# Optimization experiments

Measured on AMD Instinct MI355X. Metric: run time of the kernel, lower is better.

## Reference

```python
import jax, jax.numpy as jnp
import numpy as np

B, LC, LE, H, V = 128, 256, 257, 512, 128
PAD = 0  # padding_token_index


def lstm_cell(x, h, c, Wih, Whh, b):
    # torch LSTMCell gate order: i, f, g, o
    g = x @ Wih.T + h @ Whh.T + b
    i, f, gg, o = jnp.split(g, 4, axis=-1)
    c = jax.nn.sigmoid(f) * c + jax.nn.sigmoid(i) * jnp.tanh(gg)
    h = jax.nn.sigmoid(o) * jnp.tanh(c)
    return h, c


def setup_inputs() -> dict:
    key = jax.random.key(0)
    ks = jax.random.split(key, 32)
    p = lambda k, shape: jax.random.normal(k, shape, jnp.float32) * 0.05
    d = {
        'C_idx': jax.random.randint(ks[0], (B, LC), 0, V, dtype=jnp.int32),
        'E_idx': jax.random.randint(ks[1], (B, LE), 0, V, dtype=jnp.int32),
        'C_pad': jnp.zeros((B, LC), dtype=bool),
        'enc_Wih_f': p(ks[2], (4 * H, V)),
        'enc_Whh_f': p(ks[3], (4 * H, H)),
        'enc_b_f': p(ks[4], (4 * H,)),
        'enc_Wih_b': p(ks[5], (4 * H, V)),
        'enc_Whh_b': p(ks[6], (4 * H, H)),
        'enc_b_b': p(ks[7], (4 * H,)),
        'dec_Wih': p(ks[8], (4 * H, H + V)),
        'dec_Whh': p(ks[9], (4 * H, H)),
        'dec_b': p(ks[10], (4 * H,)),
        'Wh': p(ks[11], (H, 2 * H)),
        'Wc': p(ks[12], (H, 2 * H)),
        'Wattn': p(ks[13], (H, 2 * H)),
        'Wout': p(ks[14], (H, 3 * H)),
        'Wvocab': p(ks[15], (V, H)),
        'pg_ctx': p(ks[16], (2 * H,)),
        'pg_in': p(ks[17], (V + H,)),
        'pg_h': p(ks[18], (H,)),
        'pg_c': p(ks[19], (H,)),
        'pg_b': p(ks[20], (1,)),
    }
    return d


def _forward(C_idx, E_idx, C_pad, enc_Wih_f, enc_Whh_f, enc_b_f, enc_Wih_b, enc_Whh_b, enc_b_b,
             dec_Wih, dec_Whh, dec_b, Wh, Wc, Wattn, Wout, Wvocab,
             pg_ctx, pg_in, pg_h, pg_c, pg_b):
    C = jax.nn.one_hot(C_idx, V, dtype=jnp.float32)      # [B,LC,V]
    E_emb = jax.nn.one_hot(E_idx, V, dtype=jnp.float32)  # [B,LE,V]
    z = jnp.zeros((B, H), jnp.float32)

    xs = jnp.swapaxes(C, 0, 1)  # [LC,B,V]

    def enc_fwd(carry, x):
        h, c = lstm_cell(x, carry[0], carry[1], enc_Wih_f, enc_Whh_f, enc_b_f)
        return (h, c), h

    def enc_bwd(carry, x):
        h, c = lstm_cell(x, carry[0], carry[1], enc_Wih_b, enc_Whh_b, enc_b_b)
        return (h, c), h

    (hf, cf), Hf = jax.lax.scan(enc_fwd, (z, z), xs)
    (hb, cb), Hb = jax.lax.scan(enc_bwd, (z, z), xs[::-1])
    Hb = Hb[::-1]
    enc = jnp.swapaxes(jnp.concatenate([Hf, Hb], axis=-1), 0, 1)  # [B,LC,2H]

    # decoder init state from final encoder states (fwd;bwd concat)
    h0 = jnp.concatenate([hf, hb], axis=-1) @ Wh.T
    c0 = jnp.concatenate([cf, cb], axis=-1) @ Wc.T

    enc_proj = enc @ Wattn.T  # [B,LC,H]

    def step(carry, x_emb):
        h, c, prev_out = carry
        nin = jnp.concatenate([x_emb, prev_out], axis=1)  # [B,V+H]
        h, c = lstm_cell(nin, h, c, dec_Wih, dec_Whh, dec_b)
        scores = jnp.einsum('blh,bh->bl', enc_proj, h)
        scores = jnp.where(C_pad, -jnp.inf, scores)
        attn = jax.nn.softmax(scores, axis=1)             # [B,LC]
        ctx = jnp.einsum('bl,blh->bh', attn, enc)         # [B,2H]
        t_out = jnp.tanh(jnp.concatenate([h, ctx], axis=1) @ Wout.T)  # [B,H]
        gen = jax.nn.softmax(t_out @ Wvocab.T, axis=1)    # [B,V]
        p_gen = jax.nn.sigmoid(ctx @ pg_ctx + nin @ pg_in + h @ pg_h + c @ pg_c + pg_b[0])[:, None]
        copy_p = attn * (1.0 - p_gen)
        out = jax.vmap(lambda o, idx, a: o.at[idx].add(a))(gen * p_gen, C_idx, copy_p)
        return (h, c, t_out), out

    xs2 = jnp.swapaxes(E_emb[:, :LE - 1], 0, 1)  # teacher inputs, step 0 = start token
    _, preds = jax.lax.scan(step, (h0, c0, z), xs2)
    preds = jnp.swapaxes(preds, 0, 1)  # [B,LE-1,V]

    tgt = E_idx[:, 1:]
    nll = -jnp.take_along_axis(jnp.log(preds), tgt[..., None], axis=2)[..., 0]
    return jnp.where(tgt == PAD, 0.0, nll)  # [B,LE-1], reduction='none'


def reference(C_idx, E_idx, C_pad, enc_Wih_f, enc_Whh_f, enc_b_f, enc_Wih_b, enc_Whh_b, enc_b_b,
              dec_Wih, dec_Whh, dec_b, Wh, Wc, Wattn, Wout, Wvocab,
              pg_ctx, pg_in, pg_h, pg_c, pg_b):
    return _forward(C_idx, E_idx, C_pad, enc_Wih_f, enc_Whh_f, enc_b_f, enc_Wih_b, enc_Whh_b, enc_b_b,
                    dec_Wih, dec_Whh, dec_b, Wh, Wc, Wattn, Wout, Wvocab,
                    pg_ctx, pg_in, pg_h, pg_c, pg_b)
```

## Files before the change

### kernel.cpp

```cpp
#include <hip/hip_runtime.h>

static constexpr size_t OFF_ENC   = 0;
static constexpr size_t OFF_WGE   = 67108864;
static constexpr size_t OFF_WIHTE = 71303168;
static constexpr size_t OFF_HENC  = 72351744;
static constexpr size_t OFF_CENC  = 72876032;
static constexpr size_t OFF_WGATE = 67108864;
static constexpr size_t OFF_XDEC  = 71303168;
static constexpr size_t OFF_WATTT = 71827456;
static constexpr size_t OFF_WOUT  = 72876032;
static constexpr size_t OFF_WVOCT = 74448896;
static constexpr size_t OFF_HDEC  = 74579968;
static constexpr size_t OFF_CDEC  = 74842112;
static constexpr size_t OFF_TOUT  = 75104256;
static constexpr size_t OFF_UFB   = 75366400;
static constexpr size_t OFF_CTXF  = 75628544;
static constexpr size_t OFF_CTXP  = 75890688;
static constexpr size_t OFF_SC    = 76414976;
static constexpr size_t OFF_MSP   = 76480512;
static constexpr size_t OFF_MD    = 76482560;

__device__ __forceinline__ float sigm(float x) { return 1.f / (1.f + expf(-x)); }
__device__ __forceinline__ unsigned short f2bf(float f) {
  unsigned u = __float_as_uint(f);
  u += 0x7fffu + ((u >> 16) & 1u);
  return (unsigned short)(u >> 16);
}
__device__ __forceinline__ float bfl(unsigned w) { return __uint_as_float(w << 16); }
__device__ __forceinline__ float bfh(unsigned w) { return __uint_as_float(w & 0xffff0000u); }
__device__ __forceinline__ float bf2f(unsigned short v) { return __uint_as_float(((unsigned)v) << 16); }

#if defined(__has_builtin)
#if __has_builtin(__builtin_amdgcn_fdot2_f32_bf16)
#define HAVE_DOT2BF 1
#endif
#endif
#ifdef HAVE_DOT2BF
typedef __bf16 bf2_t __attribute__((ext_vector_type(2)));
__device__ __forceinline__ float dot2bf(unsigned w, unsigned h, float acc) {
  return __builtin_amdgcn_fdot2_f32_bf16(__builtin_bit_cast(bf2_t, w),
                                         __builtin_bit_cast(bf2_t, h), acc, false);
}
#else
__device__ __forceinline__ float dot2bf(unsigned w, unsigned h, float acc) {
  return acc + bfl(w) * bfl(h) + bfh(w) * bfh(h);
}
#endif

__global__ __launch_bounds__(256) void k_pre1(const float* __restrict__ WhhF,
                                              const float* __restrict__ WhhB,
                                              const float* __restrict__ WihF,
                                              const float* __restrict__ WihB,
                                              char* __restrict__ wsb) {
  unsigned short* WGE = (unsigned short*)(wsb + OFF_WGE);
  unsigned short* WIH = (unsigned short*)(wsb + OFF_WIHTE);
  int id = blockIdx.x * 256 + threadIdx.x, str = gridDim.x * 256;
  for (int x = id; x < 2 * 2048 * 512; x += str) {
    int dir = x >> 20, r = (x >> 9) & 2047, k = x & 511;
    const float* W = dir ? WhhB : WhhF;
    WGE[x] = f2bf(W[(size_t)r * 512 + k]);
  }
  for (int x = id; x < 2 * 128 * 2048; x += str) {
    int dir = x >> 18, v = (x >> 11) & 127, r = x & 2047;
    const float* W = dir ? WihB : WihF;
    WIH[x] = f2bf(W[(size_t)r * 128 + v]);
  }
}

__global__ __launch_bounds__(256) void k_pre2(const float* __restrict__ dWih,
                                              const float* __restrict__ dWhh,
                                              const float* __restrict__ Wattn,
                                              const float* __restrict__ Wout,
                                              const float* __restrict__ Wvoc,
                                              char* __restrict__ wsb) {
  unsigned short* WG = (unsigned short*)(wsb + OFF_WGATE);
  unsigned short* XD = (unsigned short*)(wsb + OFF_XDEC);
  unsigned short* WA = (unsigned short*)(wsb + OFF_WATTT);
  unsigned short* WO = (unsigned short*)(wsb + OFF_WOUT);
  unsigned*       WV = (unsigned*)(wsb + OFF_WVOCT);
  int id = blockIdx.x * 256 + threadIdx.x, str = gridDim.x * 256;
  for (int x = id; x < 2048 * 1024; x += str) {
    int r = x >> 10, k = x & 1023;
    float v = (k < 512) ? dWih[(size_t)r * 640 + 128 + k] : dWhh[(size_t)r * 512 + (k - 512)];
    WG[x] = f2bf(v);
  }
  for (int x = id; x < 128 * 2048; x += str) {
    int v = x >> 11, r = x & 2047;
    XD[x] = f2bf(dWih[(size_t)r * 640 + v]);
  }
  for (int x = id; x < 1024 * 512; x += str) {
    int i = x >> 9, o = x & 511;
    WA[x] = f2bf(Wattn[(size_t)o * 1024 + i]);
  }
  for (int x = id; x < 512 * 1536; x += str) WO[x] = f2bf(Wout[x]);
  for (int x = id; x < 256 * 128; x += str) {
    int kk = x >> 7, v = x & 127;
    unsigned lo = f2bf(Wvoc[(size_t)v * 512 + 2 * kk]);
    unsigned hi = f2bf(Wvoc[(size_t)v * 512 + 2 * kk + 1]);
    WV[x] = lo | (hi << 16);
  }
}

__global__ __launch_bounds__(512) void k_encs(const float* __restrict__ bF,
                                              const float* __restrict__ bB,
                                              const int* __restrict__ C_idx,
                                              char* __restrict__ wsb, int t) {
  int tau = threadIdx.x, bid = blockIdx.x;
  int b = tau & 127, slot = tau >> 7;
  int dir = bid >> 7;
  int j = __builtin_amdgcn_readfirstlane(((bid & 127) << 2) + slot);
  int dd = __builtin_amdgcn_readfirstlane(dir);
  int rp = t & 1, wp = rp ^ 1;
  const unsigned* inw = (const unsigned*)(wsb + OFF_HENC) + ((size_t)(dd * 2 + rp) * 256) * 128 + b;
  const uint4* w0 = (const uint4*)((const unsigned*)(wsb + OFF_WGE) + ((size_t)dd * 2048 + j) * 256);
  const uint4* w1 = (const uint4*)((const unsigned*)(wsb + OFF_WGE) + ((size_t)dd * 2048 + 512 + j) * 256);
  const uint4* w2 = (const uint4*)((const unsigned*)(wsb + OFF_WGE) + ((size_t)dd * 2048 + 1024 + j) * 256);
  const uint4* w3 = (const uint4*)((const unsigned*)(wsb + OFF_WGE) + ((size_t)dd * 2048 + 1536 + j) * 256);
  int l = dd ? (255 - t) : t;
  int cidx = C_idx[b * 256 + l];
  const unsigned short* xg = (const unsigned short*)(wsb + OFF_WIHTE) + ((size_t)dd * 128 + cidx) * 2048;
  const float* bias = dd ? bB : bF;
  float a0 = bias[j] + bf2f(xg[j]);
  float a1 = bias[512 + j] + bf2f(xg[512 + j]);
  float a2 = bias[1024 + j] + bf2f(xg[1024 + j]);
  float a3 = bias[1536 + j] + bf2f(xg[1536 + j]);
#pragma unroll 4
  for (int q = 0; q < 64; ++q) {
    uint4 W0 = w0[q], W1 = w1[q], W2 = w2[q], W3 = w3[q];
    unsigned i0 = inw[(q * 4 + 0) * 128], i1 = inw[(q * 4 + 1) * 128];
    unsigned i2 = inw[(q * 4 + 2) * 128], i3 = inw[(q * 4 + 3) * 128];
    a0 = dot2bf(W0.x, i0, a0); a0 = dot2bf(W0.y, i1, a0); a0 = dot2bf(W0.z, i2, a0); a0 = dot2bf(W0.w, i3, a0);
    a1 = dot2bf(W1.x, i0, a1); a1 = dot2bf(W1.y, i1, a1); a1 = dot2bf(W1.z, i2, a1); a1 = dot2bf(W1.w, i3, a1);
    a2 = dot2bf(W2.x, i0, a2); a2 = dot2bf(W2.y, i1, a2); a2 = dot2bf(W2.z, i2, a2); a2 = dot2bf(W2.w, i3, a2);
    a3 = dot2bf(W3.x, i0, a3); a3 = dot2bf(W3.y, i1, a3); a3 = dot2bf(W3.z, i2, a3); a3 = dot2bf(W3.w, i3, a3);
  }
  float ig = sigm(a0), fg = sigm(a1), gg = tanhf(a2), og = sigm(a3);
  float* cp = (float*)(wsb + OFF_CENC) + ((size_t)dir * 512 + j) * 128 + b;
  float c = fg * (*cp) + ig * gg;
  *cp = c;
  float h = og * tanhf(c);
  unsigned short hb = f2bf(h);
  ((unsigned short*)(wsb + OFF_HENC))[((((size_t)(dir * 2 + wp) * 256) + (j >> 1)) * 128 + b) * 2 + (j & 1)] = hb;
  ((unsigned short*)(wsb + OFF_ENC))[((size_t)b * 256 + l) * 1024 + dir * 512 + j] = hb;
}

__global__ __launch_bounds__(512) void k_h0(const float* __restrict__ Wh,
                                            const float* __restrict__ Wc,
                                            char* __restrict__ wsb) {
  int tau = threadIdx.x;
  int b = tau & 127, slot = tau >> 7;
  int row = __builtin_amdgcn_readfirstlane(blockIdx.x * 4 + slot);
  int sel = row >> 9, j = row & 511;
  const float* W = (sel ? Wc : Wh) + (size_t)j * 1024;
  const unsigned short* HE = (const unsigned short*)(wsb + OFF_HENC);
  const float* CE = (const float*)(wsb + OFF_CENC);
  float acc = 0.f;
  for (int k = 0; k < 1024; ++k) {
    int dir = k >> 9, k5 = k & 511;
    float in;
    if (sel == 0)
      in = bf2f(HE[((((size_t)(dir * 2 + 0) * 256) + (k5 >> 1)) * 128 + b) * 2 + (k5 & 1)]);
    else
      in = CE[((size_t)dir * 512 + k5) * 128 + b];
    acc += W[k] * in;
  }
  if (sel == 0)
    ((unsigned short*)(wsb + OFF_HDEC))[(((size_t)(j >> 1)) * 128 + b) * 2 + (j & 1)] = f2bf(acc);
  else
    ((float*)(wsb + OFF_CDEC))[(size_t)j * 128 + b] = acc;
}

__global__ __launch_bounds__(512) void k_gates(const int* __restrict__ E_idx,
                                               const float* __restrict__ db,
                                               char* __restrict__ wsb, int t) {
  __shared__ float part[2][4][128];
  int tau = threadIdx.x;
  int b = tau & 127, jslot = (tau >> 7) & 1, kh = tau >> 8;
  int j = __builtin_amdgcn_readfirstlane(blockIdx.x * 2 + jslot);
  int rp = t & 1, np = rp ^ 1;
  const unsigned* inw = (const unsigned*)(wsb + (kh ? OFF_HDEC : OFF_TOUT)) + (size_t)(kh ? np * 0 + rp : rp) * 256 * 128 + b;
  const unsigned* WG = (const unsigned*)(wsb + OFF_WGATE);
  const uint4* w0 = (const uint4*)(WG + ((size_t)(0 * 512 + j)) * 512 + kh * 256);
  const uint4* w1 = (const uint4*)(WG + ((size_t)(1 * 512 + j)) * 512 + kh * 256);
  const uint4* w2 = (const uint4*)(WG + ((size_t)(2 * 512 + j)) * 512 + kh * 256);
  const uint4* w3 = (const uint4*)(WG + ((size_t)(3 * 512 + j)) * 512 + kh * 256);
  float a0 = 0.f, a1 = 0.f, a2 = 0.f, a3 = 0.f;
#pragma unroll 4
  for (int q = 0; q < 64; ++q) {
    uint4 W0 = w0[q], W1 = w1[q], W2 = w2[q], W3 = w3[q];
    unsigned i0 = inw[(q * 4 + 0) * 128], i1 = inw[(q * 4 + 1) * 128];
    unsigned i2 = inw[(q * 4 + 2) * 128], i3 = inw[(q * 4 + 3) * 128];
    a0 = dot2bf(W0.x, i0, a0); a0 = dot2bf(W0.y, i1, a0); a0 = dot2bf(W0.z, i2, a0); a0 = dot2bf(W0.w, i3, a0);
    a1 = dot2bf(W1.x, i0, a1); a1 = dot2bf(W1.y, i1, a1); a1 = dot2bf(W1.z, i2, a1); a1 = dot2bf(W1.w, i3, a1);
    a2 = dot2bf(W2.x, i0, a2); a2 = dot2bf(W2.y, i1, a2); a2 = dot2bf(W2.z, i2, a2); a2 = dot2bf(W2.w, i3, a2);
    a3 = dot2bf(W3.x, i0, a3); a3 = dot2bf(W3.y, i1, a3); a3 = dot2bf(W3.z, i2, a3); a3 = dot2bf(W3.w, i3, a3);
  }
  if (kh == 1) { part[jslot][0][b] = a0; part[jslot][1][b] = a1; part[jslot][2][b] = a2; part[jslot][3][b] = a3; }
  __syncthreads();
  if (kh == 0) {
    int xid = E_idx[b * 257 + t];
    const unsigned short* xg = (const unsigned short*)(wsb + OFF_XDEC) + (size_t)xid * 2048;
    float g0 = a0 + part[jslot][0][b] + db[j] + bf2f(xg[j]);
    float g1 = a1 + part[jslot][1][b] + db[512 + j] + bf2f(xg[512 + j]);
    float g2 = a2 + part[jslot][2][b] + db[1024 + j] + bf2f(xg[1024 + j]);
    float g3 = a3 + part[jslot][3][b] + db[1536 + j] + bf2f(xg[1536 + j]);
    float ig = sigm(g0), fg = sigm(g1), gg = tanhf(g2), og = sigm(g3);
    float* cp = (float*)(wsb + OFF_CDEC) + (size_t)j * 128 + b;
    float c = fg * (*cp) + ig * gg;
    *cp = c;
    float h = og * tanhf(c);
    ((unsigned short*)(wsb + OFF_HDEC))[(((size_t)np * 256 + (j >> 1)) * 128 + b) * 2 + (j & 1)] = f2bf(h);
  }
}

__global__ __launch_bounds__(512) void k_u(char* __restrict__ wsb, int t) {
  int tau = threadIdx.x;
  int b = tau & 127, slot = tau >> 7;
  int i = __builtin_amdgcn_readfirstlane(blockIdx.x * 4 + slot);
  int np = (t & 1) ^ 1;
  const unsigned* inw = (const unsigned*)(wsb + OFF_HDEC) + (size_t)np * 256 * 128 + b;
  const uint4* w = (const uint4*)((const unsigned*)(wsb + OFF_WATTT) + (size_t)i * 256);
  float a = 0.f;
#pragma unroll 4
  for (int q = 0; q < 64; ++q) {
    uint4 W = w[q];
    a = dot2bf(W.x, inw[(q * 4 + 0) * 128], a);
    a = dot2bf(W.y, inw[(q * 4 + 1) * 128], a);
    a = dot2bf(W.z, inw[(q * 4 + 2) * 128], a);
    a = dot2bf(W.w, inw[(q * 4 + 3) * 128], a);
  }
  ((unsigned short*)(wsb + OFF_UFB))[(((size_t)(i >> 1)) * 128 + b) * 2 + (i & 1)] = f2bf(a);
}

__global__ __launch_bounds__(256) void k_attn(const unsigned char* __restrict__ C_pad,
                                              char* __restrict__ wsb) {
  __shared__ __align__(16) unsigned short tile[32][1024];
  __shared__ __align__(16) unsigned ulds[512];
  __shared__ float sc_l[32];
  __shared__ float p_l[32];
  __shared__ float red[4];
  int bid = blockIdx.x, tau = threadIdx.x;
  int b = bid >> 1, ch = bid & 1;
  int lane = tau & 63, wv = tau >> 6;
  const unsigned* UW = (const unsigned*)(wsb + OFF_UFB) + b;
  ulds[tau] = UW[(size_t)tau * 128];
  ulds[tau + 256] = UW[(size_t)(tau + 256) * 128];
  float mold = -3.0e38f, ssum = 0.f;
  float acc0 = 0.f, acc1 = 0.f, acc2 = 0.f, acc3 = 0.f;
  unsigned short* SCp = (unsigned short*)(wsb + OFF_SC) + (size_t)b * 256;
  int L0 = ch * 128;
  for (int sub = 0; sub < 4; ++sub) {
    const uint4* src = (const uint4*)((const unsigned short*)wsb + ((size_t)b * 256 + L0 + sub * 32) * 1024);
    __syncthreads();
#pragma unroll
    for (int it = 0; it < 16; ++it) ((uint4*)tile)[it * 256 + tau] = src[it * 256 + tau];
    __syncthreads();
    const uint4* t4 = (const uint4*)tile;
    const uint4* u4 = (const uint4*)ulds;
#pragma unroll
    for (int li = 0; li < 8; ++li) {
      int l = wv * 8 + li;
      uint4 ea = t4[l * 128 + lane * 2];
      uint4 eb = t4[l * 128 + lane * 2 + 1];
      uint4 ua = u4[lane * 2];
      uint4 ub = u4[lane * 2 + 1];
      float s = 0.f;
      s = dot2bf(ea.x, ua.x, s); s = dot2bf(ea.y, ua.y, s);
      s = dot2bf(ea.z, ua.z, s); s = dot2bf(ea.w, ua.w, s);
      s = dot2bf(eb.x, ub.x, s); s = dot2bf(eb.y, ub.y, s);
      s = dot2bf(eb.z, ub.z, s); s = dot2bf(eb.w, ub.w, s);
      for (int o = 32; o; o >>= 1) s += __shfl_xor(s, o);
      if (lane == 0) {
        int gl = L0 + sub * 32 + l;
        if (C_pad[b * 256 + gl]) s = -3.0e38f;
        sc_l[l] = s;
        SCp[gl] = f2bf(s);
      }
    }
    __syncthreads();
    if (tau < 64) {
      float v = (tau < 32) ? sc_l[tau] : -3.0e38f;
      for (int o = 32; o; o >>= 1) v = fmaxf(v, __shfl_xor(v, o));
      if (tau == 0) red[0] = v;
    }
    __syncthreads();
    float mnew = fmaxf(mold, red[0]);
    float r = expf(mold - mnew);
    if (tau < 64) {
      float pv = (tau < 32) ? expf(sc_l[tau] - mnew) : 0.f;
      if (tau < 32) p_l[tau] = pv;
      for (int o = 32; o; o >>= 1) pv += __shfl_xor(pv, o);
      if (tau == 0) red[1] = pv;
    }
    __syncthreads();
    ssum = ssum * r + red[1];
    mold = mnew;
    acc0 *= r; acc1 *= r; acc2 *= r; acc3 *= r;
    const uint2* t2 = (const uint2*)tile;
#pragma unroll 8
    for (int l = 0; l < 32; ++l) {
      float pv = p_l[l];
      uint2 ev = t2[l * 256 + tau];
      acc0 += pv * bfl(ev.x); acc1 += pv * bfh(ev.x);
      acc2 += pv * bfl(ev.y); acc3 += pv * bfh(ev.y);
    }
  }
  unsigned* CP = (unsigned*)(wsb + OFF_CTXP);
  unsigned wlo = (unsigned)f2bf(acc0) | ((unsigned)f2bf(acc1) << 16);
  unsigned whi = (unsigned)f2bf(acc2) | ((unsigned)f2bf(acc3) << 16);
  CP[(((size_t)ch * 128 + b) * 1024 + tau * 4) >> 1] = wlo;
  CP[((((size_t)ch * 128 + b) * 1024 + tau * 4) >> 1) + 1] = whi;
  if (tau == 0) {
    float* MSP = (float*)(wsb + OFF_MSP);
    MSP[b * 2 + ch] = mold;
    MSP[256 + b * 2 + ch] = ssum;
  }
}

__global__ __launch_bounds__(256) void k_comb(const int* __restrict__ E_idx,
                                              const float* __restrict__ pgc,
                                              const float* __restrict__ pgi,
                                              const float* __restrict__ pgh,
                                              const float* __restrict__ pgcc,
                                              const float* __restrict__ pgb,
                                              char* __restrict__ wsb, int t) {
  __shared__ float red[4];
  int b = blockIdx.x, tau = threadIdx.x;
  int lane = tau & 63, wv = tau >> 6;
  int rp = t & 1, np = rp ^ 1;
  const float* MSP = (const float*)(wsb + OFF_MSP);
  float m0 = MSP[b * 2], m1 = MSP[b * 2 + 1];
  float s0 = MSP[256 + b * 2], s1 = MSP[256 + b * 2 + 1];
  float M = fmaxf(m0, m1);
  float e0 = expf(m0 - M), e1 = expf(m1 - M);
  float D = s0 * e0 + s1 * e1;
  float invD = 1.f / D;
  const unsigned* CP = (const unsigned*)(wsb + OFF_CTXP);
  size_t base0 = (((size_t)0 * 128 + b) * 1024 + tau * 4) >> 1;
  size_t base1 = (((size_t)1 * 128 + b) * 1024 + tau * 4) >> 1;
  unsigned c0l = CP[base0], c0h = CP[base0 + 1], c1l = CP[base1], c1h = CP[base1 + 1];
  float x0 = (bfl(c0l) * e0 + bfl(c1l) * e1) * invD;
  float x1 = (bfh(c0l) * e0 + bfh(c1l) * e1) * invD;
  float x2 = (bfl(c0h) * e0 + bfl(c1h) * e1) * invD;
  float x3 = (bfh(c0h) * e0 + bfh(c1h) * e1) * invD;
  unsigned* CF = (unsigned*)(wsb + OFF_CTXF);
  CF[((size_t)tau * 2) * 128 + b]     = (unsigned)f2bf(x0) | ((unsigned)f2bf(x1) << 16);
  CF[((size_t)tau * 2 + 1) * 128 + b] = (unsigned)f2bf(x2) | ((unsigned)f2bf(x3) << 16);
  int f0 = tau * 4;
  float pp = x0 * pgc[f0] + x1 * pgc[f0 + 1] + x2 * pgc[f0 + 2] + x3 * pgc[f0 + 3];
  if (f0 < 512) {
    const unsigned short* H = (const unsigned short*)(wsb + OFF_HDEC);
    const unsigned short* TO = (const unsigned short*)(wsb + OFF_TOUT);
    const float* C = (const float*)(wsb + OFF_CDEC);
#pragma unroll
    for (int e = 0; e < 4; ++e) {
      int f = f0 + e;
      float hv = bf2f(H[(((size_t)np * 256 + (f >> 1)) * 128 + b) * 2 + (f & 1)]);
      float pv = bf2f(TO[(((size_t)rp * 256 + (f >> 1)) * 128 + b) * 2 + (f & 1)]);
      float cv = C[(size_t)f * 128 + b];
      pp += hv * pgh[f] + cv * pgcc[f] + pv * pgi[128 + f];
    }
  }
  for (int o = 32; o; o >>= 1) pp += __shfl_xor(pp, o);
  if (lane == 0) red[wv] = pp;
  __syncthreads();
  if (tau == 0) {
    int xid = E_idx[b * 257 + t];
    float s = red[0] + red[1] + red[2] + red[3] + pgi[xid] + pgb[0];
    float* MD = (float*)(wsb + OFF_MD);
    MD[b] = M;
    MD[128 + b] = D;
    MD[256 + b] = sigm(s);
  }
}

__global__ __launch_bounds__(512) void k_wout(char* __restrict__ wsb, int t) {
  __shared__ float part[2][128];
  int tau = threadIdx.x;
  int b = tau & 127, nslot = (tau >> 7) & 1, kh = tau >> 8;
  int n = __builtin_amdgcn_readfirstlane(blockIdx.x * 2 + nslot);
  int np = (t & 1) ^ 1;
  const unsigned* HW = (const unsigned*)(wsb + OFF_HDEC) + (size_t)np * 256 * 128 + b;
  const unsigned* CW = (const unsigned*)(wsb + OFF_CTXF) + b;
  const unsigned* w = (const unsigned*)(wsb + OFF_WOUT) + (size_t)n * 768 + kh * 384;
  float a = 0.f;
  int p0 = kh * 384;
#pragma unroll 4
  for (int q = 0; q < 96; ++q) {
    uint4 W = ((const uint4*)w)[q];
#pragma unroll
    for (int e = 0; e < 4; ++e) {
      int pp = p0 + q * 4 + e;
      unsigned in = (pp < 256) ? HW[(size_t)pp * 128] : CW[(size_t)(pp - 256) * 128];
      unsigned wv = (e == 0) ? W.x : (e == 1) ? W.y : (e == 2) ? W.z : W.w;
      a = dot2bf(wv, in, a);
    }
  }
  if (kh == 1) part[nslot][b] = a;
  __syncthreads();
  if (kh == 0) {
    float tv = tanhf(a + part[nslot][b]);
    ((unsigned short*)(wsb + OFF_TOUT))[(((size_t)np * 256 + (n >> 1)) * 128 + b) * 2 + (n & 1)] = f2bf(tv);
  }
}

__global__ __launch_bounds__(256) void k_fin(const int* __restrict__ C_idx,
                                             const int* __restrict__ E_idx,
                                             char* __restrict__ wsb,
                                             float* __restrict__ out, int t) {
  __shared__ unsigned to_pld[256];
  __shared__ float lgp[2][128];
  __shared__ float lgf[128];
  __shared__ float red[8];
  int b = blockIdx.x, tau = threadIdx.x;
  int lane = tau & 63, wv = tau >> 6;
  int np = (t & 1) ^ 1;
  const unsigned* TOW = (const unsigned*)(wsb + OFF_TOUT) + (size_t)np * 256 * 128 + b;
  to_pld[tau] = TOW[(size_t)tau * 128];
  __syncthreads();
  int v = tau & 127, kh = tau >> 7;
  const unsigned* WV = (const unsigned*)(wsb + OFF_WVOCT) + v;
  float a = 0.f;
#pragma unroll 8
  for (int kkk = 0; kkk < 128; ++kkk) {
    int kk = kh * 128 + kkk;
    a = dot2bf(WV[(size_t)kk * 128], to_pld[kk], a);
  }
  lgp[kh][v] = a;
  __syncthreads();
  if (tau < 128) {
    float lg = lgp[0][tau] + lgp[1][tau];
    lgf[tau] = lg;
    float m = lg;
    for (int o = 32; o; o >>= 1) m = fmaxf(m, __shfl_xor(m, o));
    if (lane == 0) red[wv] = m;
  }
  __syncthreads();
  float mx = fmaxf(red[0], red[1]);
  if (tau < 128) {
    float e = expf(lgf[tau] - mx);
    for (int o = 32; o; o >>= 1) e += __shfl_xor(e, o);
    if (lane == 0) red[2 + wv] = e;
  }
  __syncthreads();
  const float* MD = (const float*)(wsb + OFF_MD);
  float M = MD[b], D = MD[128 + b], pg = MD[256 + b];
  int tgt = E_idx[b * 257 + t + 1];
  float cm = 0.f;
  {
    float s = bf2f(((const unsigned short*)(wsb + OFF_SC))[(size_t)b * 256 + tau]);
    if (C_idx[b * 256 + tau] == tgt) cm = expf(s - M);
  }
  for (int o = 32; o; o >>= 1) cm += __shfl_xor(cm, o);
  if (lane == 0) red[4 + wv] = cm;
  __syncthreads();
  if (tau == 0) {
    float sume = red[2] + red[3];
    float copy_raw = red[4] + red[5] + red[6] + red[7];
    float gen_tgt = expf(lgf[tgt] - mx) / sume;
    float prob = pg * gen_tgt + (1.f - pg) * copy_raw / D;
    out[b * 256 + t] = (tgt == 0) ? 0.f : -logf(prob);
  }
}

extern "C" void kernel_launch(void* const* d_in, const int* in_sizes, int n_in,
                              void* d_out, int out_size, void* d_ws, size_t ws_size,
                              hipStream_t stream) {
  (void)in_sizes; (void)n_in; (void)out_size; (void)ws_size;
  const int* C_idx = (const int*)d_in[0];
  const int* E_idx = (const int*)d_in[1];
  const unsigned char* C_pad = (const unsigned char*)d_in[2];
  const float* eWihF = (const float*)d_in[3];
  const float* eWhhF = (const float*)d_in[4];
  const float* ebF   = (const float*)d_in[5];
  const float* eWihB = (const float*)d_in[6];
  const float* eWhhB = (const float*)d_in[7];
  const float* ebB   = (const float*)d_in[8];
  const float* dWih  = (const float*)d_in[9];
  const float* dWhh  = (const float*)d_in[10];
  const float* db    = (const float*)d_in[11];
  const float* Wh    = (const float*)d_in[12];
  const float* Wc    = (const float*)d_in[13];
  const float* Wattn = (const float*)d_in[14];
  const float* Wout  = (const float*)d_in[15];
  const float* Wvoc  = (const float*)d_in[16];
  const float* pgc   = (const float*)d_in[17];
  const float* pgi   = (const float*)d_in[18];
  const float* pgh   = (const float*)d_in[19];
  const float* pgcc  = (const float*)d_in[20];
  const float* pgb   = (const float*)d_in[21];
  char* wsb = (char*)d_ws;
  float* out = (float*)d_out;

  hipMemsetAsync(wsb + OFF_HENC, 0, 524288, stream);
  hipMemsetAsync(wsb + OFF_CENC, 0, 524288, stream);
  hipMemsetAsync(wsb + OFF_TOUT, 0, 262144, stream);

  k_pre1<<<256, 256, 0, stream>>>(eWhhF, eWhhB, eWihF, eWihB, wsb);
  for (int t = 0; t < 256; ++t)
    k_encs<<<256, 512, 0, stream>>>(ebF, ebB, C_idx, wsb, t);
  k_h0<<<256, 512, 0, stream>>>(Wh, Wc, wsb);
  k_pre2<<<256, 256, 0, stream>>>(dWih, dWhh, Wattn, Wout, Wvoc, wsb);
  for (int t = 0; t < 256; ++t) {
    k_gates<<<256, 512, 0, stream>>>(E_idx, db, wsb, t);
    k_u<<<256, 512, 0, stream>>>(wsb, t);
    k_attn<<<256, 256, 0, stream>>>(C_pad, wsb);
    k_comb<<<128, 256, 0, stream>>>(E_idx, pgc, pgi, pgh, pgcc, pgb, wsb, t);
    k_wout<<<256, 512, 0, stream>>>(wsb, t);
    k_fin<<<128, 256, 0, stream>>>(C_idx, E_idx, wsb, out, t);
  }
}
```

Baseline: 27.29 ms.

## Replace per-step encoder launches with one persistent kernel per batch-direction

The 256 per-timestep encoder launches are replaced by a single kernel in which each block owns one (batch, direction) pair and runs the whole recurrence, keeping h in shared memory and c in registers. Encoder weights are repacked so each thread reads its four gate weights for a pair of k values as one 16-byte load. This removes launch overhead and global round-trips of the hidden state each step. In exchange, only 256 blocks each stream the full 2 MB recurrent weight matrix every step, so performance rests on L2 bandwidth and a serial per-block dependency chain.

```diff
diff --git a/kernel.cpp b/kernel.cpp
--- a/kernel.cpp
+++ b/kernel.cpp
@@ -52,19 +52,91 @@
                                               const float* __restrict__ WihF,
                                               const float* __restrict__ WihB,
                                               char* __restrict__ wsb) {
-  unsigned short* WGE = (unsigned short*)(wsb + OFF_WGE);
-  unsigned short* WIH = (unsigned short*)(wsb + OFF_WIHTE);
+  unsigned short* dst = (unsigned short*)(wsb + OFF_WGE);
   int id = blockIdx.x * 256 + threadIdx.x, str = gridDim.x * 256;
-  for (int x = id; x < 2 * 2048 * 512; x += str) {
-    int dir = x >> 20, r = (x >> 9) & 2047, k = x & 511;
+  for (int x = id; x < 2097152; x += str) {
+    int dir = x >> 20, r = x & 1048575;
+    int e = r & 7, j = (r >> 3) & 511, k2 = r >> 12;
+    int g = e >> 1, k = k2 * 2 + (e & 1);
     const float* W = dir ? WhhB : WhhF;
-    WGE[x] = f2bf(W[(size_t)r * 512 + k]);
-  }
-  for (int x = id; x < 2 * 128 * 2048; x += str) {
-    int dir = x >> 18, v = (x >> 11) & 127, r = x & 2047;
+    dst[x] = f2bf(W[((size_t)g * 512 + j) * 512 + k]);
+  }
+  for (int x = id; x < 524288; x += str) {
+    int dir = x >> 18, r = x & 262143;
+    int g = r & 3, j = (r >> 2) & 511, v = r >> 11;
     const float* W = dir ? WihB : WihF;
-    WIH[x] = f2bf(W[(size_t)r * 128 + v]);
-  }
+    dst[2097152 + x] = f2bf(W[((size_t)g * 512 + j) * 128 + v]);
+  }
+}
+
+__global__ __launch_bounds__(512) void k_enc(const float* __restrict__ bF,
+                                             const float* __restrict__ bB,
+                                             const int* __restrict__ C_idx,
+                                             char* __restrict__ wsb) {
+  __shared__ __align__(16) unsigned short hbf[512];
+  int bid = blockIdx.x;
+  int b = bid & 127, dir = bid >> 7;
+  int j = threadIdx.x;
+  const unsigned short* WH = (const unsigned short*)(wsb + OFF_WGE) + (size_t)dir * 1048576;
+  const unsigned short* WX = (const unsigned short*)(wsb + OFF_WGE) + 2097152 + (size_t)dir * 262144;
+  const float* bias = dir ? bB : bF;
+  float b0 = bias[j], b1 = bias[512 + j], b2 = bias[1024 + j], b3 = bias[1536 + j];
+  unsigned short* encb = (unsigned short*)wsb + (size_t)b * 262144;
+  const uint4* wp = (const uint4*)WH + j;
+  float c = 0.f, h = 0.f;
+  hbf[j] = 0;
+  __syncthreads();
+  for (int t = 0; t < 256; ++t) {
+    int l = dir ? (255 - t) : t;
+    int cidx = C_idx[b * 256 + l];
+    uint2 xg = *(const uint2*)(WX + ((size_t)cidx * 512 + j) * 4);
+    float a0 = b0 + bfl(xg.x), a1 = b1 + bfh(xg.x);
+    float a2 = b2 + bfl(xg.y), a3 = b3 + bfh(xg.y);
+    for (int k2 = 0; k2 < 256; ++k2) {
+      uint4 w = wp[(size_t)k2 * 512];
+      unsigned hp = *(const unsigned*)((const char*)hbf + k2 * 4);
+      a0 = dot2bf(w.x, hp, a0);
+      a1 = dot2bf(w.y, hp, a1);
+      a2 = dot2bf(w.z, hp, a2);
+      a3 = dot2bf(w.w, hp, a3);
+    }
+    float ig = sigm(a0), fg = sigm(a1), gg = tanhf(a2), og = sigm(a3);
+    c = fg * c + ig * gg;
+    h = og * tanhf(c);
+    __syncthreads();
+    unsigned short hb = f2bf(h);
+    hbf[j] = hb;
+    encb[(size_t)l * 1024 + dir * 512 + j] = hb;
+    __syncthreads();
+  }
+  ((unsigned short*)(wsb + OFF_HENC))[(((size_t)(dir * 2 + 0) * 256 + (j >> 1)) * 128 + b) * 2 + (j & 1)] = f2bf(h);
+  ((float*)(wsb + OFF_CENC))[((size_t)dir * 512 + j) * 128 + b] = c;
+}
+
+__global__ __launch_bounds__(512) void k_h0(const float* __restrict__ Wh,
+                                            const float* __restrict__ Wc,
+                                            char* __restrict__ wsb) {
+  int tau = threadIdx.x;
+  int b = tau & 127, slot = tau >> 7;
+  int row = __builtin_amdgcn_readfirstlane(blockIdx.x * 4 + slot);
+  int sel = row >> 9, j = row & 511;
+  const float* W = (sel ? Wc : Wh) + (size_t)j * 1024;
+  const unsigned short* HE = (const unsigned short*)(wsb + OFF_HENC);
+  const float* CE = (const float*)(wsb + OFF_CENC);
+  float acc = 0.f;
+  for (int k = 0; k < 1024; ++k) {
+    int dir = k >> 9, k5 = k & 511;
+    float in;
+    if (sel == 0)
+      in = bf2f(HE[(((size_t)(dir * 2 + 0) * 256 + (k5 >> 1)) * 128 + b) * 2 + (k5 & 1)]);
+    else
+      in = CE[((size_t)dir * 512 + k5) * 128 + b];
+    acc += W[k] * in;
+  }
+  if (sel == 0)
+    ((unsigned short*)(wsb + OFF_HDEC))[(((size_t)(j >> 1)) * 128 + b) * 2 + (j & 1)] = f2bf(acc);
+  else
+    ((float*)(wsb + OFF_CDEC))[(size_t)j * 128 + b] = acc;
 }
 
 __global__ __launch_bounds__(256) void k_pre2(const float* __restrict__ dWih,
@@ -101,75 +173,6 @@
   }
 }
 
-__global__ __launch_bounds__(512) void k_encs(const float* __restrict__ bF,
-                                              const float* __restrict__ bB,
-                                              const int* __restrict__ C_idx,
-                                              char* __restrict__ wsb, int t) {
-  int tau = threadIdx.x, bid = blockIdx.x;
-  int b = tau & 127, slot = tau >> 7;
-  int dir = bid >> 7;
-  int j = __builtin_amdgcn_readfirstlane(((bid & 127) << 2) + slot);
-  int dd = __builtin_amdgcn_readfirstlane(dir);
-  int rp = t & 1, wp = rp ^ 1;
-  const unsigned* inw = (const unsigned*)(wsb + OFF_HENC) + ((size_t)(dd * 2 + rp) * 256) * 128 + b;
-  const uint4* w0 = (const uint4*)((const unsigned*)(wsb + OFF_WGE) + ((size_t)dd * 2048 + j) * 256);
-  const uint4* w1 = (const uint4*)((const unsigned*)(wsb + OFF_WGE) + ((size_t)dd * 2048 + 512 + j) * 256);
-  const uint4* w2 = (const uint4*)((const unsigned*)(wsb + OFF_WGE) + ((size_t)dd * 2048 + 1024 + j) * 256);
-  const uint4* w3 = (const uint4*)((const unsigned*)(wsb + OFF_WGE) + ((size_t)dd * 2048 + 1536 + j) * 256);
-  int l = dd ? (255 - t) : t;
-  int cidx = C_idx[b * 256 + l];
-  const unsigned short* xg = (const unsigned short*)(wsb + OFF_WIHTE) + ((size_t)dd * 128 + cidx) * 2048;
-  const float* bias = dd ? bB : bF;
-  float a0 = bias[j] + bf2f(xg[j]);
-  float a1 = bias[512 + j] + bf2f(xg[512 + j]);
-  float a2 = bias[1024 + j] + bf2f(xg[1024 + j]);
-  float a3 = bias[1536 + j] + bf2f(xg[1536 + j]);
-#pragma unroll 4
-  for (int q = 0; q < 64; ++q) {
-    uint4 W0 = w0[q], W1 = w1[q], W2 = w2[q], W3 = w3[q];
-    unsigned i0 = inw[(q * 4 + 0) * 128], i1 = inw[(q * 4 + 1) * 128];
-    unsigned i2 = inw[(q * 4 + 2) * 128], i3 = inw[(q * 4 + 3) * 128];
-    a0 = dot2bf(W0.x, i0, a0); a0 = dot2bf(W0.y, i1, a0); a0 = dot2bf(W0.z, i2, a0); a0 = dot2bf(W0.w, i3, a0);
-    a1 = dot2bf(W1.x, i0, a1); a1 = dot2bf(W1.y, i1, a1); a1 = dot2bf(W1.z, i2, a1); a1 = dot2bf(W1.w, i3, a1);
-    a2 = dot2bf(W2.x, i0, a2); a2 = dot2bf(W2.y, i1, a2); a2 = dot2bf(W2.z, i2, a2); a2 = dot2bf(W2.w, i3, a2);
-    a3 = dot2bf(W3.x, i0, a3); a3 = dot2bf(W3.y, i1, a3); a3 = dot2bf(W3.z, i2, a3); a3 = dot2bf(W3.w, i3, a3);
-  }
-  float ig = sigm(a0), fg = sigm(a1), gg = tanhf(a2), og = sigm(a3);
-  float* cp = (float*)(wsb + OFF_CENC) + ((size_t)dir * 512 + j) * 128 + b;
-  float c = fg * (*cp) + ig * gg;
-  *cp = c;
-  float h = og * tanhf(c);
-  unsigned short hb = f2bf(h);
-  ((unsigned short*)(wsb + OFF_HENC))[((((size_t)(dir * 2 + wp) * 256) + (j >> 1)) * 128 + b) * 2 + (j & 1)] = hb;
-  ((unsigned short*)(wsb + OFF_ENC))[((size_t)b * 256 + l) * 1024 + dir * 512 + j] = hb;
-}
-
-__global__ __launch_bounds__(512) void k_h0(const float* __restrict__ Wh,
-                                            const float* __restrict__ Wc,
-                                            char* __restrict__ wsb) {
-  int tau = threadIdx.x;
-  int b = tau & 127, slot = tau >> 7;
-  int row = __builtin_amdgcn_readfirstlane(blockIdx.x * 4 + slot);
-  int sel = row >> 9, j = row & 511;
-  const float* W = (sel ? Wc : Wh) + (size_t)j * 1024;
-  const unsigned short* HE = (const unsigned short*)(wsb + OFF_HENC);
-  const float* CE = (const float*)(wsb + OFF_CENC);
-  float acc = 0.f;
-  for (int k = 0; k < 1024; ++k) {
-    int dir = k >> 9, k5 = k & 511;
-    float in;
-    if (sel == 0)
-      in = bf2f(HE[((((size_t)(dir * 2 + 0) * 256) + (k5 >> 1)) * 128 + b) * 2 + (k5 & 1)]);
-    else
-      in = CE[((size_t)dir * 512 + k5) * 128 + b];
-    acc += W[k] * in;
-  }
-  if (sel == 0)
-    ((unsigned short*)(wsb + OFF_HDEC))[(((size_t)(j >> 1)) * 128 + b) * 2 + (j & 1)] = f2bf(acc);
-  else
-    ((float*)(wsb + OFF_CDEC))[(size_t)j * 128 + b] = acc;
-}
-
 __global__ __launch_bounds__(512) void k_gates(const int* __restrict__ E_idx,
                                                const float* __restrict__ db,
                                                char* __restrict__ wsb, int t) {
@@ -178,12 +181,12 @@
   int b = tau & 127, jslot = (tau >> 7) & 1, kh = tau >> 8;
   int j = __builtin_amdgcn_readfirstlane(blockIdx.x * 2 + jslot);
   int rp = t & 1, np = rp ^ 1;
-  const unsigned* inw = (const unsigned*)(wsb + (kh ? OFF_HDEC : OFF_TOUT)) + (size_t)(kh ? np * 0 + rp : rp) * 256 * 128 + b;
+  const unsigned* inw = (const unsigned*)(wsb + (kh ? OFF_HDEC : OFF_TOUT)) + (size_t)rp * 32768 + b;
   const unsigned* WG = (const unsigned*)(wsb + OFF_WGATE);
-  const uint4* w0 = (const uint4*)(WG + ((size_t)(0 * 512 + j)) * 512 + kh * 256);
-  const uint4* w1 = (const uint4*)(WG + ((size_t)(1 * 512 + j)) * 512 + kh * 256);
-  const uint4* w2 = (const uint4*)(WG + ((size_t)(2 * 512 + j)) * 512 + kh * 256);
-  const uint4* w3 = (const uint4*)(WG + ((size_t)(3 * 512 + j)) * 512 + kh * 256);
+  const uint4* w0 = (const uint4*)(WG + (size_t)j * 512 + kh * 256);
+  const uint4* w1 = (const uint4*)(WG + ((size_t)512 + j) * 512 + kh * 256);
+  const uint4* w2 = (const uint4*)(WG + ((size_t)1024 + j) * 512 + kh * 256);
+  const uint4* w3 = (const uint4*)(WG + ((size_t)1536 + j) * 512 + kh * 256);
   float a0 = 0.f, a1 = 0.f, a2 = 0.f, a3 = 0.f;
 #pragma unroll 4
   for (int q = 0; q < 64; ++q) {
@@ -218,7 +221,7 @@
   int b = tau & 127, slot = tau >> 7;
   int i = __builtin_amdgcn_readfirstlane(blockIdx.x * 4 + slot);
   int np = (t & 1) ^ 1;
-  const unsigned* inw = (const unsigned*)(wsb + OFF_HDEC) + (size_t)np * 256 * 128 + b;
+  const unsigned* inw = (const unsigned*)(wsb + OFF_HDEC) + (size_t)np * 32768 + b;
   const uint4* w = (const uint4*)((const unsigned*)(wsb + OFF_WATTT) + (size_t)i * 256);
   float a = 0.f;
 #pragma unroll 4
@@ -380,7 +383,7 @@
   int b = tau & 127, nslot = (tau >> 7) & 1, kh = tau >> 8;
   int n = __builtin_amdgcn_readfirstlane(blockIdx.x * 2 + nslot);
   int np = (t & 1) ^ 1;
-  const unsigned* HW = (const unsigned*)(wsb + OFF_HDEC) + (size_t)np * 256 * 128 + b;
+  const unsigned* HW = (const unsigned*)(wsb + OFF_HDEC) + (size_t)np * 32768 + b;
   const unsigned* CW = (const unsigned*)(wsb + OFF_CTXF) + b;
   const unsigned* w = (const unsigned*)(wsb + OFF_WOUT) + (size_t)n * 768 + kh * 384;
   float a = 0.f;
@@ -415,7 +418,7 @@
   int b = blockIdx.x, tau = threadIdx.x;
   int lane = tau & 63, wv = tau >> 6;
   int np = (t & 1) ^ 1;
-  const unsigned* TOW = (const unsigned*)(wsb + OFF_TOUT) + (size_t)np * 256 * 128 + b;
+  const unsigned* TOW = (const unsigned*)(wsb + OFF_TOUT) + (size_t)np * 32768 + b;
   to_pld[tau] = TOW[(size_t)tau * 128];
   __syncthreads();
   int v = tau & 127, kh = tau >> 7;
@@ -492,13 +495,10 @@
   char* wsb = (char*)d_ws;
   float* out = (float*)d_out;
 
-  hipMemsetAsync(wsb + OFF_HENC, 0, 524288, stream);
-  hipMemsetAsync(wsb + OFF_CENC, 0, 524288, stream);
   hipMemsetAsync(wsb + OFF_TOUT, 0, 262144, stream);
 
   k_pre1<<<256, 256, 0, stream>>>(eWhhF, eWhhB, eWihF, eWihB, wsb);
-  for (int t = 0; t < 256; ++t)
-    k_encs<<<256, 512, 0, stream>>>(ebF, ebB, C_idx, wsb, t);
+  k_enc<<<256, 512, 0, stream>>>(ebF, ebB, C_idx, wsb);
   k_h0<<<256, 512, 0, stream>>>(Wh, Wc, wsb);
   k_pre2<<<256, 256, 0, stream>>>(dWih, dWhh, Wattn, Wout, Wvoc, wsb);
   for (int t = 0; t < 256; ++t) {
```

Result: slower. 28.24 ms (+3.5%).
